# Kernel optimization log

Hardware: AMD Instinct MI355X
Metric: run time of the kernel (lower is better)

The kernel has to match this reference:

```python
import jax, jax.numpy as jnp
import numpy as np

NB_KERNEL = 16
NUM_POS_EMB = 16
DMAX = 20.0


def _grbf_encode(d):
    # d: (..., ) distances; centers 0..DMAX in NB_KERNEL steps (matches torch.arange(0, 20*(1+1/15), 20/15))
    centers = jnp.linspace(0.0, DMAX, NB_KERNEL, dtype=jnp.float32)
    return jnp.exp(-jnp.square(d[..., None] - centers))


def _positional_embeddings(d):
    # d: (..., ) float offsets
    freq = jnp.exp(jnp.arange(0, NUM_POS_EMB, 2, dtype=jnp.float32) * (-(np.log(10000.0) / NUM_POS_EMB)))
    angles = d[..., None] * freq  # (..., NUM_POS_EMB//2)
    return jnp.concatenate([jnp.cos(angles), jnp.sin(angles)], axis=-1)


def setup_inputs() -> dict:
    key = jax.random.key(0)
    # coordinates in Angstrom-ish scale so pairwise distances span the RBF range
    crd = jax.random.normal(key, (4096, 4, 3), dtype=jnp.float32) * 10.0
    return {"crd": crd, "max_neigh": 64}


def reference(crd, max_neigh):
    nb_var = crd.shape[0]
    nb_neigh = min(max_neigh, nb_var - 1)

    # virtual Cbeta atom from backbone geometry
    b = crd[:, 1] - crd[:, 0]
    c = crd[:, 2] - crd[:, 1]
    a = jnp.cross(b, c)
    Cb = -0.58273431 * a + 0.56802827 * b - 0.54067466 * c + crd[:, 1]
    crd5 = jnp.concatenate([crd, Cb[:, None, :]], axis=1)  # (N, 5, 3)

    # pairwise CA distances, diagonal forced to -1 so self sorts first
    ca = crd5[:, 1]  # (N, 3)
    D = jnp.linalg.norm(ca[:, None, :] - ca[None, :, :], axis=-1)  # (N, N)
    diag = jnp.arange(nb_var)
    D = D.at[diag, diag].set(-1.0)

    # nb_neigh smallest distances (= top_k of -D); self is column 0
    neg_d, idx_pairs = jax.lax.top_k(-D, nb_neigh)  # (N, K)
    d = -neg_d
    d = d.at[:, 0].set(0.0)
    d = jnp.nan_to_num(d, nan=0.0)

    # all-pairs atom distances between residue i (5 atoms) and each neighbor j (5 atoms)
    neigh = crd5[idx_pairs]  # (N, K, 5, 3)
    diff = crd5[:, None, :, None, :] - neigh[:, :, None, :, :]  # (N, K, 5, 5, 3); [i,k,a,b]=crd[i,a]-crd[j,b]
    dist = jnp.linalg.norm(diff, axis=-1).reshape(nb_var, nb_neigh, 25)
    dist = _grbf_encode(dist).reshape(nb_var, nb_neigh, 25 * NB_KERNEL)
    dist = jnp.nan_to_num(dist, nan=0.0)

    # sinusoidal encoding of sequence-index offsets
    offsets = jnp.abs(diag[:, None] - idx_pairs).astype(jnp.float32)  # (N, K)
    pos = _positional_embeddings(offsets)  # (N, K, NUM_POS_EMB)

    return (d, dist, pos, idx_pairs)
```

## Files before the change

kernel.cpp:

```cpp
#include <hip/hip_runtime.h>
#include <math.h>

#define NBV 4096
#define KNE 64
#define D_OFF    0
#define DIST_OFF (NBV*KNE)
#define POS_OFF  (DIST_OFF + NBV*KNE*400)
#define IDX_OFF  (POS_OFF + NBV*KNE*16)

#define WS_CRD5 0
#define WS_CA4  (NBV*16)
#define WS_JIDX (NBV*20)
#define WS_FLOATS (NBV*20 + NBV*KNE)

typedef float f4v __attribute__((ext_vector_type(4)));

__device__ __forceinline__ unsigned int f2sort(float f) {
  unsigned int u = __float_as_uint(f);
  return (u & 0x80000000u) ? ~u : (u | 0x80000000u);
}
__device__ __forceinline__ float sort2f(unsigned int s) {
  unsigned int u = (s & 0x80000000u) ? (s & 0x7FFFFFFFu) : ~s;
  return __uint_as_float(u);
}

__device__ __forceinline__ float4 crd5_f4(const float* __restrict__ crd, int r,
                                          int q) {
  if (q < 3) return ((const float4*)crd)[r * 3 + q];
  const float4 a = ((const float4*)crd)[r * 3 + 0];
  const float4 b = ((const float4*)crd)[r * 3 + 1];
  const float4 c = ((const float4*)crd)[r * 3 + 2];
  const float bx = a.w - a.x, by = b.x - a.y, bz = b.y - a.z;
  const float cx = b.z - a.w, cy = b.w - b.x, cz = c.x - b.y;
  const float axv = by * cz - bz * cy;
  const float ayv = bz * cx - bx * cz;
  const float azv = bx * cy - by * cx;
  return make_float4(
      -0.58273431f * axv + 0.56802827f * bx - 0.54067466f * cx + a.w,
      -0.58273431f * ayv + 0.56802827f * by - 0.54067466f * cy + b.x,
      -0.58273431f * azv + 0.56802827f * bz - 0.54067466f * cz + b.y, 0.0f);
}

__global__ __launch_bounds__(256) void prep_k(const float* __restrict__ crd,
                                              float* __restrict__ ws) {
  const int r = blockIdx.x * 256 + threadIdx.x;
  const float4 a = ((const float4*)crd)[r * 3 + 0];
  const float4 b = ((const float4*)crd)[r * 3 + 1];
  const float4 c = ((const float4*)crd)[r * 3 + 2];
  const float bx = a.w - a.x, by = b.x - a.y, bz = b.y - a.z;
  const float cx = b.z - a.w, cy = b.w - b.x, cz = c.x - b.y;
  const float axv = by * cz - bz * cy;
  const float ayv = bz * cx - bx * cz;
  const float azv = bx * cy - by * cx;
  const float cbx = -0.58273431f * axv + 0.56802827f * bx - 0.54067466f * cx + a.w;
  const float cby = -0.58273431f * ayv + 0.56802827f * by - 0.54067466f * cy + b.x;
  const float cbz = -0.58273431f * azv + 0.56802827f * bz - 0.54067466f * cz + b.y;

  float4* row = (float4*)(ws + WS_CRD5 + r * 16);
  row[0] = a;
  row[1] = b;
  row[2] = c;
  row[3] = make_float4(cbx, cby, cbz, 0.0f);
  ((float4*)(ws + WS_CA4))[r] = make_float4(a.w, b.x, b.y, 0.0f);
}

__global__ __launch_bounds__(256) void selA_k(const float* __restrict__ ws,
                                              float* __restrict__ out,
                                              int* __restrict__ jidx_ws) {
  const int i = blockIdx.x;
  const int t = threadIdx.x;

  __shared__ unsigned int hist[2048];
  __shared__ unsigned long long cand[512];
  __shared__ int jidx[64];
  __shared__ unsigned int cnt;
  __shared__ int selbin;
  __shared__ unsigned int wsum[4];

  for (int b = t; b < 2048; b += 256) hist[b] = 0u;
  if (t == 0) cnt = 0u;
  __syncthreads();

  const float4 ci = ((const float4*)(ws + WS_CA4))[i];

  float dv[16];
#pragma unroll
  for (int s = 0; s < 16; s++) {
    const int j = t + 256 * s;
    const float4 cj = ((const float4*)(ws + WS_CA4))[j];
    const float dx = ci.x - cj.x, dy = ci.y - cj.y, dz = ci.z - cj.z;
    float f = sqrtf(dx * dx + dy * dy + dz * dz);
    if (j == i) f = -1.0f;
    dv[s] = f;
    int b = (int)(f * 16.0f);
    b = b < 0 ? 0 : (b > 2047 ? 2047 : b);
    atomicAdd(&hist[b], 1u);
  }
  __syncthreads();

  unsigned int bc[8];
  unsigned int loc = 0;
#pragma unroll
  for (int r = 0; r < 8; r++) { bc[r] = hist[t * 8 + r]; loc += bc[r]; }
  const int lane = t & 63, wid = t >> 6;
  unsigned int x = loc;
#pragma unroll
  for (int off = 1; off < 64; off <<= 1) {
    unsigned int y = __shfl_up(x, off, 64);
    if (lane >= off) x += y;
  }
  if (lane == 63) wsum[wid] = x;
  __syncthreads();
  unsigned int woff = 0;
#pragma unroll
  for (int w = 0; w < 4; w++)
    if (w < wid) woff += wsum[w];
  unsigned int c = woff + x - loc;
#pragma unroll
  for (int r = 0; r < 8; r++) {
    if (c < 64u && c + bc[r] >= 64u) selbin = t * 8 + r;
    c += bc[r];
  }
  __syncthreads();
  const int B = selbin;

#pragma unroll
  for (int s = 0; s < 16; s++) {
    const float f = dv[s];
    int b = (int)(f * 16.0f);
    b = b < 0 ? 0 : (b > 2047 ? 2047 : b);
    if (b <= B) {
      const unsigned int p = atomicAdd(&cnt, 1u);
      if (p < 512u) {
        const int j = t + 256 * s;
        cand[p] = (((unsigned long long)f2sort(f)) << 32) | (unsigned int)j;
      }
    }
  }
  __syncthreads();
  unsigned int M = cnt;
  if (M > 512u) M = 512u;
  for (int p = t; p < 512; p += 256)
    if ((unsigned)p >= M) cand[p] = 0xFFFFFFFFFFFFFFFFull;

  int P = 64;
  while (P < (int)M) P <<= 1;
  for (int ksz = 2; ksz <= P; ksz <<= 1) {
    for (int jsz = ksz >> 1; jsz > 0; jsz >>= 1) {
      __syncthreads();
      if (t < (P >> 1)) {
        const int a = ((t & ~(jsz - 1)) << 1) | (t & (jsz - 1));
        const int b2 = a | jsz;
        const unsigned long long va = cand[a], vb = cand[b2];
        const bool up = ((a & ksz) == 0);
        if ((va > vb) == up) { cand[a] = vb; cand[b2] = va; }
      }
    }
  }
  __syncthreads();

  if (t < KNE) {
    const unsigned long long key = cand[t];
    const int j = (int)(unsigned int)(key & 0xFFFFFFFFull);
    const float f = sort2f((unsigned int)(key >> 32));
    jidx[t] = j;
    jidx_ws[i * KNE + t] = j;
    out[D_OFF + i * KNE + t] = (t == 0) ? 0.0f : f;
    out[IDX_OFF + i * KNE + t] = (float)j;
  }
  __syncthreads();

  {
    const int n = t >> 2, g = t & 3;
    const int j = jidx[n];
    int di = i - j;
    if (di < 0) di = -di;
    const float offv = (float)di;
    const bool hi = (g & 1);
    const float fA = hi ? 0.01f                   : 1.0f;
    const float fB = hi ? 0.0031622776601683794f  : 0.31622776601683794f;
    const float fC = hi ? 0.001f                  : 0.1f;
    const float fD = hi ? 0.00031622776601683794f : 0.031622776601683791f;
    float s0, c0, s1, c1, s2, c2, s3, c3;
    sincosf(offv * fA, &s0, &c0);
    sincosf(offv * fB, &s1, &c1);
    sincosf(offv * fC, &s2, &c2);
    sincosf(offv * fD, &s3, &c3);
    f4v o;
    if (g < 2) o = (f4v){c0, c1, c2, c3};
    else       o = (f4v){s0, s1, s2, s3};
    f4v* pv = (f4v*)(out + POS_OFF) + (size_t)(i * KNE + n) * 4 + g;
    __builtin_nontemporal_store(o, pv);
  }
}

__global__ __launch_bounds__(256) void distB_k(const float* __restrict__ ws,
                                               const int* __restrict__ jidx_ws,
                                               float* __restrict__ out) {
  const int i = blockIdx.x;
  const int t = threadIdx.x;

  __shared__ float rows[65 * 16];
  __shared__ float dvals[1600];
  __shared__ int jidx[64];

  if (t < 64) jidx[t] = jidx_ws[i * KNE + t];
  __syncthreads();

  {
    const int sr = t >> 2, qq = t & 3;
    ((float4*)rows)[sr * 4 + qq] = ((const float4*)ws)[jidx[sr] * 4 + qq];
    if (t < 4) ((float4*)rows)[64 * 4 + t] = ((const float4*)ws)[i * 4 + t];
  }
  __syncthreads();

#pragma unroll
  for (int it = 0; it < 7; it++) {
    const int pid = t + 256 * it;
    if (pid < 1600) {
      const int k = pid / 25;
      const int p = pid - k * 25;
      const int p0 = p / 5;
      const int p1 = p - p0 * 5;
      const float dx = rows[64 * 16 + p0 * 3 + 0] - rows[k * 16 + p1 * 3 + 0];
      const float dy = rows[64 * 16 + p0 * 3 + 1] - rows[k * 16 + p1 * 3 + 1];
      const float dz = rows[64 * 16 + p0 * 3 + 2] - rows[k * 16 + p1 * 3 + 2];
      dvals[pid] = sqrtf(dx * dx + dy * dy + dz * dz);
    }
  }
  __syncthreads();

  const float step = 20.0f / 15.0f;
  const float TWO_S = 2.6666667f;
  const float S2 = 1.7777778f;
  const float RHO = 0.02856550f;
  f4v* dst = (f4v*)(out + DIST_OFF) + (size_t)i * 6400;
#pragma unroll
  for (int s = 0; s < 25; s++) {
    const int f4i = t + 256 * s;
    const int pair = f4i >> 2;
    const float cb0 = (float)((f4i & 3) * 4) * step;
    float u = dvals[pair] - cb0;
    u = fminf(u, 16.0f);
    float e = __expf(-u * u);
    float q = __expf(fmaf(TWO_S, u, -S2));
    f4v o;
    o.x = e;
    e *= q;           o.y = e;
    q *= RHO; e *= q; o.z = e;
    q *= RHO; e *= q; o.w = e;
    __builtin_nontemporal_store(o, dst + f4i);
  }
}

template <bool USE_WS>
__global__ __launch_bounds__(256) void fused_k(const float* __restrict__ crd,
                                               const float* __restrict__ ws,
                                               float* __restrict__ out) {
  const int i = blockIdx.x;
  const int t = threadIdx.x;

  __shared__ float region0[2688];
  __shared__ unsigned long long cand[512];
  __shared__ int jidx[64];
  __shared__ unsigned int cnt;
  __shared__ int selbin;
  __shared__ unsigned int wsum[4];

  unsigned int* hist = (unsigned int*)region0;
  float* rows = region0;
  float* dvals = region0 + 1040;

  for (int b = t; b < 2048; b += 256) hist[b] = 0u;
  if (t == 0) cnt = 0u;
  __syncthreads();

  float cax, cay, caz;
  cax = crd[i * 12 + 3]; cay = crd[i * 12 + 4]; caz = crd[i * 12 + 5];

  float dv[16];
#pragma unroll
  for (int s = 0; s < 16; s++) {
    const int j = t + 256 * s;
    float jx = crd[j * 12 + 3], jy = crd[j * 12 + 4], jz = crd[j * 12 + 5];
    const float dx = cax - jx, dy = cay - jy, dz = caz - jz;
    float f = sqrtf(dx * dx + dy * dy + dz * dz);
    if (j == i) f = -1.0f;
    dv[s] = f;
    int b = (int)(f * 16.0f);
    b = b < 0 ? 0 : (b > 2047 ? 2047 : b);
    atomicAdd(&hist[b], 1u);
  }
  __syncthreads();

  unsigned int bc[8];
  unsigned int loc = 0;
#pragma unroll
  for (int r = 0; r < 8; r++) { bc[r] = hist[t * 8 + r]; loc += bc[r]; }
  const int lane = t & 63, wid = t >> 6;
  unsigned int x = loc;
#pragma unroll
  for (int off = 1; off < 64; off <<= 1) {
    unsigned int y = __shfl_up(x, off, 64);
    if (lane >= off) x += y;
  }
  if (lane == 63) wsum[wid] = x;
  __syncthreads();
  unsigned int woff = 0;
#pragma unroll
  for (int w = 0; w < 4; w++)
    if (w < wid) woff += wsum[w];
  unsigned int c = woff + x - loc;
#pragma unroll
  for (int r = 0; r < 8; r++) {
    if (c < 64u && c + bc[r] >= 64u) selbin = t * 8 + r;
    c += bc[r];
  }
  __syncthreads();
  const int B = selbin;

#pragma unroll
  for (int s = 0; s < 16; s++) {
    const float f = dv[s];
    int b = (int)(f * 16.0f);
    b = b < 0 ? 0 : (b > 2047 ? 2047 : b);
    if (b <= B) {
      const unsigned int p = atomicAdd(&cnt, 1u);
      if (p < 512u) {
        const int j = t + 256 * s;
        cand[p] = (((unsigned long long)f2sort(f)) << 32) | (unsigned int)j;
      }
    }
  }
  __syncthreads();
  unsigned int M = cnt;
  if (M > 512u) M = 512u;
  for (int p = t; p < 512; p += 256)
    if ((unsigned)p >= M) cand[p] = 0xFFFFFFFFFFFFFFFFull;

  int P = 64;
  while (P < (int)M) P <<= 1;
  for (int ksz = 2; ksz <= P; ksz <<= 1) {
    for (int jsz = ksz >> 1; jsz > 0; jsz >>= 1) {
      __syncthreads();
      if (t < (P >> 1)) {
        const int a = ((t & ~(jsz - 1)) << 1) | (t & (jsz - 1));
        const int b2 = a | jsz;
        const unsigned long long va = cand[a], vb = cand[b2];
        const bool up = ((a & ksz) == 0);
        if ((va > vb) == up) { cand[a] = vb; cand[b2] = va; }
      }
    }
  }
  __syncthreads();

  if (t < KNE) {
    const unsigned long long key = cand[t];
    const int j = (int)(unsigned int)(key & 0xFFFFFFFFull);
    const float f = sort2f((unsigned int)(key >> 32));
    jidx[t] = j;
    out[D_OFF + i * KNE + t] = (t == 0) ? 0.0f : f;
    out[IDX_OFF + i * KNE + t] = (float)j;
  }
  __syncthreads();

  const int sr = t >> 2, qq = t & 3;
  float4 v, v2;
  v = crd5_f4(crd, jidx[sr], qq);
  if (t < 4) v2 = crd5_f4(crd, i, t);

  {
    const int n = sr, g = qq;
    const int j = jidx[n];
    int di = i - j;
    if (di < 0) di = -di;
    const float offv = (float)di;
    const bool hi = (g & 1);
    const float fA = hi ? 0.01f                   : 1.0f;
    const float fB = hi ? 0.0031622776601683794f  : 0.31622776601683794f;
    const float fC = hi ? 0.001f                  : 0.1f;
    const float fD = hi ? 0.00031622776601683794f : 0.031622776601683791f;
    float s0, c0, s1, c1, s2, c2, s3, c3;
    sincosf(offv * fA, &s0, &c0);
    sincosf(offv * fB, &s1, &c1);
    sincosf(offv * fC, &s2, &c2);
    sincosf(offv * fD, &s3, &c3);
    f4v o;
    if (g < 2) o = (f4v){c0, c1, c2, c3};
    else       o = (f4v){s0, s1, s2, s3};
    f4v* pv = (f4v*)(out + POS_OFF) + (size_t)(i * KNE + n) * 4 + g;
    __builtin_nontemporal_store(o, pv);
  }

  ((float4*)rows)[sr * 4 + qq] = v;
  if (t < 4) ((float4*)rows)[64 * 4 + t] = v2;
  __syncthreads();

#pragma unroll
  for (int it = 0; it < 7; it++) {
    const int pid = t + 256 * it;
    if (pid < 1600) {
      const int k = pid / 25;
      const int p = pid - k * 25;
      const int p0 = p / 5;
      const int p1 = p - p0 * 5;
      const float dx = rows[64 * 16 + p0 * 3 + 0] - rows[k * 16 + p1 * 3 + 0];
      const float dy = rows[64 * 16 + p0 * 3 + 1] - rows[k * 16 + p1 * 3 + 1];
      const float dz = rows[64 * 16 + p0 * 3 + 2] - rows[k * 16 + p1 * 3 + 2];
      dvals[pid] = sqrtf(dx * dx + dy * dy + dz * dz);
    }
  }
  __syncthreads();

  const float step = 20.0f / 15.0f;
  const float TWO_S = 2.6666667f;
  const float S2 = 1.7777778f;
  const float RHO = 0.02856550f;
  f4v* dst = (f4v*)(out + DIST_OFF) + (size_t)i * 6400;
#pragma unroll
  for (int s = 0; s < 25; s++) {
    const int f4i = t + 256 * s;
    const int pair = f4i >> 2;
    const float cb0 = (float)((f4i & 3) * 4) * step;
    float u = dvals[pair] - cb0;
    u = fminf(u, 16.0f);
    float e = __expf(-u * u);
    float q = __expf(fmaf(TWO_S, u, -S2));
    f4v o;
    o.x = e;
    e *= q;           o.y = e;
    q *= RHO; e *= q; o.z = e;
    q *= RHO; e *= q; o.w = e;
    __builtin_nontemporal_store(o, dst + f4i);
  }
}

extern "C" void kernel_launch(void* const* d_in, const int* in_sizes, int n_in,
                              void* d_out, int out_size, void* d_ws, size_t ws_size,
                              hipStream_t stream) {
  const float* crd = (const float*)d_in[0];
  float* out = (float*)d_out;
  if (ws_size >= (size_t)WS_FLOATS * sizeof(float)) {
    float* ws = (float*)d_ws;
    int* jidx_ws = (int*)(ws + WS_JIDX);
    hipLaunchKernelGGL(prep_k, dim3(NBV / 256), dim3(256), 0, stream, crd, ws);
    hipLaunchKernelGGL(selA_k, dim3(NBV), dim3(256), 0, stream, ws, out,
                       jidx_ws);
    hipLaunchKernelGGL(distB_k, dim3(NBV), dim3(256), 0, stream, ws, jidx_ws,
                       out);
  } else {
    hipLaunchKernelGGL(fused_k<false>, dim3(NBV), dim3(256), 0, stream, crd,
                       (const float*)nullptr, out);
  }
}
```

Baseline: 472.6 us.

## Fuse selection and RBF kernels into persistent multi-row blocks with overlapped distance pass

Replaces the separate selection and distance/RBF kernels with one kernel in which each block handles four residues. The next residue's CA distances and histogram are computed inside the current residue's RBF store loop, so compute overlaps the large output stores. Candidate compaction now uses a wave ballot with one atomic per wave instead of one per thread. The bitonic sort is replaced by a rank-by-counting selection. Together these remove a kernel launch and the neighbour-index workspace round trip, at the cost of fewer blocks and an O(M^2) rank loop.

```diff
diff --git a/kernel.cpp b/kernel.cpp
--- a/kernel.cpp
+++ b/kernel.cpp
@@ -3,6 +3,8 @@
 
 #define NBV 4096
 #define KNE 64
+#define RPB 4
+#define NBLK (NBV/RPB)
 #define D_OFF    0
 #define DIST_OFF (NBV*KNE)
 #define POS_OFF  (DIST_OFF + NBV*KNE*400)
@@ -10,8 +12,7 @@
 
 #define WS_CRD5 0
 #define WS_CA4  (NBV*16)
-#define WS_JIDX (NBV*20)
-#define WS_FLOATS (NBV*20 + NBV*KNE)
+#define WS_FLOATS (NBV*16 + NBV*4)
 
 typedef float f4v __attribute__((ext_vector_type(4)));
 
@@ -64,31 +65,230 @@
   ((float4*)(ws + WS_CA4))[r] = make_float4(a.w, b.x, b.y, 0.0f);
 }
 
-__global__ __launch_bounds__(256) void selA_k(const float* __restrict__ ws,
-                                              float* __restrict__ out,
-                                              int* __restrict__ jidx_ws) {
+__global__ __launch_bounds__(256) void fused_p(const float* __restrict__ ws,
+                                               float* __restrict__ out) {
+  const int t = threadIdx.x;
+  const int lane = t & 63, wid = t >> 6;
+  const unsigned long long lmask = (1ull << lane) - 1ull;
+
+  __shared__ unsigned int hist[2048];
+  __shared__ unsigned long long cand[512];
+  __shared__ float rowsd[2640];
+  __shared__ int jidx[64];
+  __shared__ unsigned int cnt;
+  __shared__ int selbin;
+  __shared__ unsigned int wsum[4];
+
+  float* rows = rowsd;
+  float* dvals = rowsd + 1040;
+
+  for (int b = t; b < 2048; b += 256) hist[b] = 0u;
+  __syncthreads();
+
+  float dv[16];
+  {
+    const int i = blockIdx.x;
+    const float4 ci = ((const float4*)(ws + WS_CA4))[i];
+#pragma unroll
+    for (int s = 0; s < 16; s++) {
+      const int j = t + 256 * s;
+      const float4 cj = ((const float4*)(ws + WS_CA4))[j];
+      const float dx = ci.x - cj.x, dy = ci.y - cj.y, dz = ci.z - cj.z;
+      float f = sqrtf(dx * dx + dy * dy + dz * dz);
+      if (j == i) f = -1.0f;
+      dv[s] = f;
+      int b = (int)(f * 16.0f);
+      b = b < 0 ? 0 : (b > 2047 ? 2047 : b);
+      atomicAdd(&hist[b], 1u);
+    }
+  }
+
+  for (int rr = 0; rr < RPB; rr++) {
+    const int i = blockIdx.x + NBLK * rr;
+    __syncthreads();
+
+    unsigned int bc[8];
+    unsigned int loc = 0;
+#pragma unroll
+    for (int r = 0; r < 8; r++) { bc[r] = hist[t * 8 + r]; loc += bc[r]; }
+    unsigned int x = loc;
+#pragma unroll
+    for (int off = 1; off < 64; off <<= 1) {
+      unsigned int y = __shfl_up(x, off, 64);
+      if (lane >= off) x += y;
+    }
+    if (lane == 63) wsum[wid] = x;
+    if (t == 0) cnt = 0u;
+    __syncthreads();
+    unsigned int woff = 0;
+#pragma unroll
+    for (int w = 0; w < 4; w++)
+      if (w < wid) woff += wsum[w];
+    unsigned int cum = woff + x - loc;
+#pragma unroll
+    for (int r = 0; r < 8; r++) {
+      if (cum < 64u && cum + bc[r] >= 64u) selbin = t * 8 + r;
+      cum += bc[r];
+    }
+    __syncthreads();
+    const int B = selbin;
+
+#pragma unroll
+    for (int s = 0; s < 16; s++) {
+      const float f = dv[s];
+      int b = (int)(f * 16.0f);
+      b = b < 0 ? 0 : (b > 2047 ? 2047 : b);
+      const bool pred = (b <= B);
+      const unsigned long long mask = __ballot(pred);
+      unsigned int base = 0;
+      if (lane == 0 && mask)
+        base = atomicAdd(&cnt, (unsigned int)__popcll(mask));
+      base = __shfl(base, 0, 64);
+      if (pred) {
+        const unsigned int p = base + (unsigned int)__popcll(mask & lmask);
+        if (p < 512u) {
+          const int j = t + 256 * s;
+          cand[p] = (((unsigned long long)f2sort(f)) << 32) | (unsigned int)j;
+        }
+      }
+    }
+    __syncthreads();
+
+    {
+      unsigned int M = cnt;
+      if (M > 512u) M = 512u;
+      for (int p = t; p < (int)M; p += 256) {
+        const unsigned long long key = cand[p];
+        int r = 0;
+        for (int q = 0; q < (int)M; q++) r += (cand[q] < key);
+        if (r < KNE) {
+          const int j = (int)(unsigned int)(key & 0xFFFFFFFFull);
+          const float f = sort2f((unsigned int)(key >> 32));
+          jidx[r] = j;
+          out[D_OFF + (size_t)i * KNE + r] = (r == 0) ? 0.0f : f;
+          out[IDX_OFF + (size_t)i * KNE + r] = (float)j;
+        }
+      }
+    }
+    for (int b = t; b < 2048; b += 256) hist[b] = 0u;
+    __syncthreads();
+
+    const int sr = t >> 2, qq = t & 3;
+    float4 v = ((const float4*)ws)[jidx[sr] * 4 + qq];
+    float4 v2;
+    if (t < 4) v2 = ((const float4*)ws)[i * 4 + t];
+
+    {
+      const int n = sr, g = qq;
+      const int j = jidx[n];
+      int di = i - j;
+      if (di < 0) di = -di;
+      const float offv = (float)di;
+      const bool hi = (g & 1);
+      const float fA = hi ? 0.01f                   : 1.0f;
+      const float fB = hi ? 0.0031622776601683794f  : 0.31622776601683794f;
+      const float fC = hi ? 0.001f                  : 0.1f;
+      const float fD = hi ? 0.00031622776601683794f : 0.031622776601683791f;
+      float s0, c0, s1, c1, s2, c2, s3, c3;
+      sincosf(offv * fA, &s0, &c0);
+      sincosf(offv * fB, &s1, &c1);
+      sincosf(offv * fC, &s2, &c2);
+      sincosf(offv * fD, &s3, &c3);
+      f4v o;
+      if (g < 2) o = (f4v){c0, c1, c2, c3};
+      else       o = (f4v){s0, s1, s2, s3};
+      f4v* pv = (f4v*)(out + POS_OFF) + ((size_t)i * KNE + n) * 4 + g;
+      __builtin_nontemporal_store(o, pv);
+    }
+
+    ((float4*)rows)[sr * 4 + qq] = v;
+    if (t < 4) ((float4*)rows)[64 * 4 + t] = v2;
+    __syncthreads();
+
+#pragma unroll
+    for (int it = 0; it < 7; it++) {
+      const int pid = t + 256 * it;
+      if (pid < 1600) {
+        const int k = pid / 25;
+        const int p = pid - k * 25;
+        const int p0 = p / 5;
+        const int p1 = p - p0 * 5;
+        const float dx = rows[64 * 16 + p0 * 3 + 0] - rows[k * 16 + p1 * 3 + 0];
+        const float dy = rows[64 * 16 + p0 * 3 + 1] - rows[k * 16 + p1 * 3 + 1];
+        const float dz = rows[64 * 16 + p0 * 3 + 2] - rows[k * 16 + p1 * 3 + 2];
+        dvals[pid] = sqrtf(dx * dx + dy * dy + dz * dz);
+      }
+    }
+    __syncthreads();
+
+    const bool nxt = (rr + 1 < RPB);
+    const int inext = blockIdx.x + NBLK * (rr + 1);
+    float4 cin = make_float4(0.0f, 0.0f, 0.0f, 0.0f);
+    if (nxt) cin = ((const float4*)(ws + WS_CA4))[inext];
+    const float step = 20.0f / 15.0f;
+    const float TWO_S = 2.6666667f;
+    const float S2 = 1.7777778f;
+    const float RHO = 0.02856550f;
+    f4v* dst = (f4v*)(out + DIST_OFF) + (size_t)i * 6400;
+#pragma unroll
+    for (int s = 0; s < 25; s++) {
+      const int f4i = t + 256 * s;
+      const int pair = f4i >> 2;
+      const float cb0 = (float)((f4i & 3) * 4) * step;
+      float u = dvals[pair] - cb0;
+      u = fminf(u, 16.0f);
+      float e = __expf(-u * u);
+      float q = __expf(fmaf(TWO_S, u, -S2));
+      f4v o;
+      o.x = e;
+      e *= q;           o.y = e;
+      q *= RHO; e *= q; o.z = e;
+      q *= RHO; e *= q; o.w = e;
+      __builtin_nontemporal_store(o, dst + f4i);
+      if (nxt && s < 16) {
+        const int j = t + 256 * s;
+        const float4 cj = ((const float4*)(ws + WS_CA4))[j];
+        const float dx = cin.x - cj.x, dy = cin.y - cj.y, dz = cin.z - cj.z;
+        float f = sqrtf(dx * dx + dy * dy + dz * dz);
+        if (j == inext) f = -1.0f;
+        dv[s] = f;
+        int b = (int)(f * 16.0f);
+        b = b < 0 ? 0 : (b > 2047 ? 2047 : b);
+        atomicAdd(&hist[b], 1u);
+      }
+    }
+  }
+}
+
+__global__ __launch_bounds__(256) void fused_k(const float* __restrict__ crd,
+                                               float* __restrict__ out) {
   const int i = blockIdx.x;
   const int t = threadIdx.x;
 
-  __shared__ unsigned int hist[2048];
+  __shared__ float region0[2688];
   __shared__ unsigned long long cand[512];
   __shared__ int jidx[64];
   __shared__ unsigned int cnt;
   __shared__ int selbin;
   __shared__ unsigned int wsum[4];
 
+  unsigned int* hist = (unsigned int*)region0;
+  float* rows = region0;
+  float* dvals = region0 + 1040;
+
   for (int b = t; b < 2048; b += 256) hist[b] = 0u;
   if (t == 0) cnt = 0u;
   __syncthreads();
 
-  const float4 ci = ((const float4*)(ws + WS_CA4))[i];
+  const float cax = crd[i * 12 + 3], cay = crd[i * 12 + 4],
+              caz = crd[i * 12 + 5];
 
   float dv[16];
 #pragma unroll
   for (int s = 0; s < 16; s++) {
     const int j = t + 256 * s;
-    const float4 cj = ((const float4*)(ws + WS_CA4))[j];
-    const float dx = ci.x - cj.x, dy = ci.y - cj.y, dz = ci.z - cj.z;
+    const float dx = cax - crd[j * 12 + 3], dy = cay - crd[j * 12 + 4],
+                dz = caz - crd[j * 12 + 5];
     float f = sqrtf(dx * dx + dy * dy + dz * dz);
     if (j == i) f = -1.0f;
     dv[s] = f;
@@ -124,243 +324,43 @@
   __syncthreads();
   const int B = selbin;
 
+  const unsigned long long lmask = (1ull << lane) - 1ull;
 #pragma unroll
   for (int s = 0; s < 16; s++) {
     const float f = dv[s];
     int b = (int)(f * 16.0f);
     b = b < 0 ? 0 : (b > 2047 ? 2047 : b);
-    if (b <= B) {
-      const unsigned int p = atomicAdd(&cnt, 1u);
-      if (p < 512u) {
+    const bool pred = (b <= B);
+    const unsigned long long mask = __ballot(pred);
+    unsigned int base = 0;
+    if (lane == 0 && mask)
+      base = atomicAdd(&cnt, (unsigned int)__popcll(mask));
+    base = __shfl(base, 0, 64);
+    if (pred) {
+      const unsigned int pp = base + (unsigned int)__popcll(mask & lmask);
+      if (pp < 512u) {
         const int j = t + 256 * s;
-        cand[p] = (((unsigned long long)f2sort(f)) << 32) | (unsigned int)j;
-      }
-    }
-  }
-  __syncthreads();
-  unsigned int M = cnt;
-  if (M > 512u) M = 512u;
-  for (int p = t; p < 512; p += 256)
-    if ((unsigned)p >= M) cand[p] = 0xFFFFFFFFFFFFFFFFull;
-
-  int P = 64;
-  while (P < (int)M) P <<= 1;
-  for (int ksz = 2; ksz <= P; ksz <<= 1) {
-    for (int jsz = ksz >> 1; jsz > 0; jsz >>= 1) {
-      __syncthreads();
-      if (t < (P >> 1)) {
-        const int a = ((t & ~(jsz - 1)) << 1) | (t & (jsz - 1));
-        const int b2 = a | jsz;
-        const unsigned long long va = cand[a], vb = cand[b2];
-        const bool up = ((a & ksz) == 0);
-        if ((va > vb) == up) { cand[a] = vb; cand[b2] = va; }
-      }
-    }
-  }
-  __syncthreads();
-
-  if (t < KNE) {
-    const unsigned long long key = cand[t];
-    const int j = (int)(unsigned int)(key & 0xFFFFFFFFull);
-    const float f = sort2f((unsigned int)(key >> 32));
-    jidx[t] = j;
-    jidx_ws[i * KNE + t] = j;
-    out[D_OFF + i * KNE + t] = (t == 0) ? 0.0f : f;
-    out[IDX_OFF + i * KNE + t] = (float)j;
+        cand[pp] = (((unsigned long long)f2sort(f)) << 32) | (unsigned int)j;
+      }
+    }
   }
   __syncthreads();
 
   {
-    const int n = t >> 2, g = t & 3;
-    const int j = jidx[n];
-    int di = i - j;
-    if (di < 0) di = -di;
-    const float offv = (float)di;
-    const bool hi = (g & 1);
-    const float fA = hi ? 0.01f                   : 1.0f;
-    const float fB = hi ? 0.0031622776601683794f  : 0.31622776601683794f;
-    const float fC = hi ? 0.001f                  : 0.1f;
-    const float fD = hi ? 0.00031622776601683794f : 0.031622776601683791f;
-    float s0, c0, s1, c1, s2, c2, s3, c3;
-    sincosf(offv * fA, &s0, &c0);
-    sincosf(offv * fB, &s1, &c1);
-    sincosf(offv * fC, &s2, &c2);
-    sincosf(offv * fD, &s3, &c3);
-    f4v o;
-    if (g < 2) o = (f4v){c0, c1, c2, c3};
-    else       o = (f4v){s0, s1, s2, s3};
-    f4v* pv = (f4v*)(out + POS_OFF) + (size_t)(i * KNE + n) * 4 + g;
-    __builtin_nontemporal_store(o, pv);
-  }
-}
-
-__global__ __launch_bounds__(256) void distB_k(const float* __restrict__ ws,
-                                               const int* __restrict__ jidx_ws,
-                                               float* __restrict__ out) {
-  const int i = blockIdx.x;
-  const int t = threadIdx.x;
-
-  __shared__ float rows[65 * 16];
-  __shared__ float dvals[1600];
-  __shared__ int jidx[64];
-
-  if (t < 64) jidx[t] = jidx_ws[i * KNE + t];
-  __syncthreads();
-
-  {
-    const int sr = t >> 2, qq = t & 3;
-    ((float4*)rows)[sr * 4 + qq] = ((const float4*)ws)[jidx[sr] * 4 + qq];
-    if (t < 4) ((float4*)rows)[64 * 4 + t] = ((const float4*)ws)[i * 4 + t];
-  }
-  __syncthreads();
-
-#pragma unroll
-  for (int it = 0; it < 7; it++) {
-    const int pid = t + 256 * it;
-    if (pid < 1600) {
-      const int k = pid / 25;
-      const int p = pid - k * 25;
-      const int p0 = p / 5;
-      const int p1 = p - p0 * 5;
-      const float dx = rows[64 * 16 + p0 * 3 + 0] - rows[k * 16 + p1 * 3 + 0];
-      const float dy = rows[64 * 16 + p0 * 3 + 1] - rows[k * 16 + p1 * 3 + 1];
-      const float dz = rows[64 * 16 + p0 * 3 + 2] - rows[k * 16 + p1 * 3 + 2];
-      dvals[pid] = sqrtf(dx * dx + dy * dy + dz * dz);
-    }
-  }
-  __syncthreads();
-
-  const float step = 20.0f / 15.0f;
-  const float TWO_S = 2.6666667f;
-  const float S2 = 1.7777778f;
-  const float RHO = 0.02856550f;
-  f4v* dst = (f4v*)(out + DIST_OFF) + (size_t)i * 6400;
-#pragma unroll
-  for (int s = 0; s < 25; s++) {
-    const int f4i = t + 256 * s;
-    const int pair = f4i >> 2;
-    const float cb0 = (float)((f4i & 3) * 4) * step;
-    float u = dvals[pair] - cb0;
-    u = fminf(u, 16.0f);
-    float e = __expf(-u * u);
-    float q = __expf(fmaf(TWO_S, u, -S2));
-    f4v o;
-    o.x = e;
-    e *= q;           o.y = e;
-    q *= RHO; e *= q; o.z = e;
-    q *= RHO; e *= q; o.w = e;
-    __builtin_nontemporal_store(o, dst + f4i);
-  }
-}
-
-template <bool USE_WS>
-__global__ __launch_bounds__(256) void fused_k(const float* __restrict__ crd,
-                                               const float* __restrict__ ws,
-                                               float* __restrict__ out) {
-  const int i = blockIdx.x;
-  const int t = threadIdx.x;
-
-  __shared__ float region0[2688];
-  __shared__ unsigned long long cand[512];
-  __shared__ int jidx[64];
-  __shared__ unsigned int cnt;
-  __shared__ int selbin;
-  __shared__ unsigned int wsum[4];
-
-  unsigned int* hist = (unsigned int*)region0;
-  float* rows = region0;
-  float* dvals = region0 + 1040;
-
-  for (int b = t; b < 2048; b += 256) hist[b] = 0u;
-  if (t == 0) cnt = 0u;
-  __syncthreads();
-
-  float cax, cay, caz;
-  cax = crd[i * 12 + 3]; cay = crd[i * 12 + 4]; caz = crd[i * 12 + 5];
-
-  float dv[16];
-#pragma unroll
-  for (int s = 0; s < 16; s++) {
-    const int j = t + 256 * s;
-    float jx = crd[j * 12 + 3], jy = crd[j * 12 + 4], jz = crd[j * 12 + 5];
-    const float dx = cax - jx, dy = cay - jy, dz = caz - jz;
-    float f = sqrtf(dx * dx + dy * dy + dz * dz);
-    if (j == i) f = -1.0f;
-    dv[s] = f;
-    int b = (int)(f * 16.0f);
-    b = b < 0 ? 0 : (b > 2047 ? 2047 : b);
-    atomicAdd(&hist[b], 1u);
-  }
-  __syncthreads();
-
-  unsigned int bc[8];
-  unsigned int loc = 0;
-#pragma unroll
-  for (int r = 0; r < 8; r++) { bc[r] = hist[t * 8 + r]; loc += bc[r]; }
-  const int lane = t & 63, wid = t >> 6;
-  unsigned int x = loc;
-#pragma unroll
-  for (int off = 1; off < 64; off <<= 1) {
-    unsigned int y = __shfl_up(x, off, 64);
-    if (lane >= off) x += y;
-  }
-  if (lane == 63) wsum[wid] = x;
-  __syncthreads();
-  unsigned int woff = 0;
-#pragma unroll
-  for (int w = 0; w < 4; w++)
-    if (w < wid) woff += wsum[w];
-  unsigned int c = woff + x - loc;
-#pragma unroll
-  for (int r = 0; r < 8; r++) {
-    if (c < 64u && c + bc[r] >= 64u) selbin = t * 8 + r;
-    c += bc[r];
-  }
-  __syncthreads();
-  const int B = selbin;
-
-#pragma unroll
-  for (int s = 0; s < 16; s++) {
-    const float f = dv[s];
-    int b = (int)(f * 16.0f);
-    b = b < 0 ? 0 : (b > 2047 ? 2047 : b);
-    if (b <= B) {
-      const unsigned int p = atomicAdd(&cnt, 1u);
-      if (p < 512u) {
-        const int j = t + 256 * s;
-        cand[p] = (((unsigned long long)f2sort(f)) << 32) | (unsigned int)j;
-      }
-    }
-  }
-  __syncthreads();
-  unsigned int M = cnt;
-  if (M > 512u) M = 512u;
-  for (int p = t; p < 512; p += 256)
-    if ((unsigned)p >= M) cand[p] = 0xFFFFFFFFFFFFFFFFull;
-
-  int P = 64;
-  while (P < (int)M) P <<= 1;
-  for (int ksz = 2; ksz <= P; ksz <<= 1) {
-    for (int jsz = ksz >> 1; jsz > 0; jsz >>= 1) {
-      __syncthreads();
-      if (t < (P >> 1)) {
-        const int a = ((t & ~(jsz - 1)) << 1) | (t & (jsz - 1));
-        const int b2 = a | jsz;
-        const unsigned long long va = cand[a], vb = cand[b2];
-        const bool up = ((a & ksz) == 0);
-        if ((va > vb) == up) { cand[a] = vb; cand[b2] = va; }
-      }
-    }
-  }
-  __syncthreads();
-
-  if (t < KNE) {
-    const unsigned long long key = cand[t];
-    const int j = (int)(unsigned int)(key & 0xFFFFFFFFull);
-    const float f = sort2f((unsigned int)(key >> 32));
-    jidx[t] = j;
-    out[D_OFF + i * KNE + t] = (t == 0) ? 0.0f : f;
-    out[IDX_OFF + i * KNE + t] = (float)j;
+    unsigned int M = cnt;
+    if (M > 512u) M = 512u;
+    for (int pi = t; pi < (int)M; pi += 256) {
+      const unsigned long long key = cand[pi];
+      int r = 0;
+      for (int q = 0; q < (int)M; q++) r += (cand[q] < key);
+      if (r < KNE) {
+        const int j = (int)(unsigned int)(key & 0xFFFFFFFFull);
+        const float f = sort2f((unsigned int)(key >> 32));
+        jidx[r] = j;
+        out[D_OFF + i * KNE + r] = (r == 0) ? 0.0f : f;
+        out[IDX_OFF + i * KNE + r] = (float)j;
+      }
+    }
   }
   __syncthreads();
 
@@ -442,14 +442,9 @@
   float* out = (float*)d_out;
   if (ws_size >= (size_t)WS_FLOATS * sizeof(float)) {
     float* ws = (float*)d_ws;
-    int* jidx_ws = (int*)(ws + WS_JIDX);
     hipLaunchKernelGGL(prep_k, dim3(NBV / 256), dim3(256), 0, stream, crd, ws);
-    hipLaunchKernelGGL(selA_k, dim3(NBV), dim3(256), 0, stream, ws, out,
-                       jidx_ws);
-    hipLaunchKernelGGL(distB_k, dim3(NBV), dim3(256), 0, stream, ws, jidx_ws,
-                       out);
+    hipLaunchKernelGGL(fused_p, dim3(NBLK), dim3(256), 0, stream, ws, out);
   } else {
-    hipLaunchKernelGGL(fused_k<false>, dim3(NBV), dim3(256), 0, stream, crd,
-                       (const float*)nullptr, out);
-  }
-}
+    hipLaunchKernelGGL(fused_k, dim3(NBV), dim3(256), 0, stream, crd, out);
+  }
+}
```

Result: no change. 471.4 us (-0.3%).
